# Optimization experiments

Hardware: AMD Instinct MI355X
Metric: run time of the kernel (lower is better)

Reference implementation:

```python
import jax, jax.numpy as jnp
import numpy as np

N = 64          # num_nodes (EEG electrodes)
T = 200         # time steps
B = 64          # batch
H = 64          # hidden_dim
K = 3           # cheb_k
F_IN = 1        # input_dim
D_GRU = 2 * H * N  # 8192, GRU input size


def setup_inputs() -> dict:
    key = jax.random.key(0)
    ks = jax.random.split(key, 24)
    s = 0.05
    inp = {
        "x": jax.random.normal(ks[0], (B, N, T), dtype=jnp.float32),
        "spatial_ei": jax.random.randint(ks[1], (2, 512), 0, N, dtype=jnp.int32),
        "spatial_ew": jax.random.uniform(ks[2], (512,), dtype=jnp.float32),
        "functional_ei": jax.random.randint(ks[3], (2, 1024), 0, N, dtype=jnp.int32),
        "functional_ew": jax.random.uniform(ks[4], (1024,), dtype=jnp.float32),
        # ChebConv: K separate Linear(F_IN->H, bias shared once)
        "Wcheb": jax.random.normal(ks[5], (K, F_IN, H), dtype=jnp.float32) * s,
        "bcheb": jnp.zeros((H,), jnp.float32),
        # GCNConv
        "Wgcn": jax.random.normal(ks[6], (F_IN, H), dtype=jnp.float32) * s,
        "bgcn": jnp.zeros((H,), jnp.float32),
        # bidirectional GRU (torch layout: gates r,z,n stacked -> 3H rows)
        "Wih_f": jax.random.normal(ks[7], (3 * H, D_GRU), dtype=jnp.float32) * s,
        "Whh_f": jax.random.normal(ks[8], (3 * H, H), dtype=jnp.float32) * s,
        "bih_f": jnp.zeros((3 * H,), jnp.float32),
        "bhh_f": jnp.zeros((3 * H,), jnp.float32),
        "Wih_b": jax.random.normal(ks[9], (3 * H, D_GRU), dtype=jnp.float32) * s,
        "Whh_b": jax.random.normal(ks[10], (3 * H, H), dtype=jnp.float32) * s,
        "bih_b": jnp.zeros((3 * H,), jnp.float32),
        "bhh_b": jnp.zeros((3 * H,), jnp.float32),
        # attention + classifier heads
        "attn_W": jax.random.normal(ks[11], (2 * H, 1), dtype=jnp.float32) * s,
        "attn_b": jnp.zeros((1,), jnp.float32),
        "clf_W": jax.random.normal(ks[12], (2 * H, 1), dtype=jnp.float32) * s,
        "clf_b": jnp.zeros((1,), jnp.float32),
    }
    return inp


def _gru_scan(xp, Whh, bhh, reverse):
    # xp: [B, T, 3H] precomputed input projection; returns [B, T, H]
    xp_t = jnp.swapaxes(xp, 0, 1)  # [T, B, 3H]
    Hh = Whh.shape[1]

    def step(h, xg):
        hg = h @ Whh.T + bhh
        xr, xz, xn = jnp.split(xg, 3, axis=-1)
        hr, hz, hn = jnp.split(hg, 3, axis=-1)
        r = jax.nn.sigmoid(xr + hr)
        z = jax.nn.sigmoid(xz + hz)
        n = jnp.tanh(xn + r * hn)
        h_new = (1.0 - z) * n + z * h
        return h_new, h_new

    h0 = jnp.zeros((xp.shape[0], Hh), xp.dtype)
    _, hs = jax.lax.scan(step, h0, xp_t, reverse=reverse)
    return jnp.swapaxes(hs, 0, 1)


def _forward(x, spatial_ei, spatial_ew, functional_ei, functional_ew,
             Wcheb, bcheb, Wgcn, bgcn,
             Wih_f, Whh_f, bih_f, bhh_f, Wih_b, Whh_b, bih_b, bhh_b,
             attn_W, attn_b, clf_W, clf_b):
    x = x[..., None]  # [B, N, T, 1] (the x.dim()==3 -> unsqueeze path)
    Bsz, Nn, Tt, _ = x.shape

    # ---- ChebConv (PyG, sym norm, lambda_max=2): L_tilde = -D^-1/2 A D^-1/2
    # (scaled-Laplacian self loops cancel: 2*1/2 - 1 = 0)
    row, col = spatial_ei[0], spatial_ei[1]
    deg = jax.ops.segment_sum(spatial_ew, row, num_segments=Nn)
    dinv = jnp.where(deg > 0, jax.lax.rsqrt(jnp.where(deg > 0, deg, 1.0)), 0.0)
    wn = dinv[row] * spatial_ew * dinv[col]
    # operator S[i, j]: aggregate source j into target i (source_to_target flow)
    S = jnp.zeros((Nn, Nn), x.dtype).at[col, row].add(wn)
    Ltil = -S
    Tx0 = x
    Tx1 = jnp.einsum('ij,bjtf->bitf', Ltil, Tx0)
    out_s = jnp.einsum('bntf,fh->bnth', Tx0, Wcheb[0]) + jnp.einsum('bntf,fh->bnth', Tx1, Wcheb[1])
    for k in range(2, K):
        Tx2 = 2.0 * jnp.einsum('ij,bjtf->bitf', Ltil, Tx1) - Tx0
        out_s = out_s + jnp.einsum('bntf,fh->bnth', Tx2, Wcheb[k])
        Tx0, Tx1 = Tx1, Tx2
    h_sp = out_s + bcheb  # [B, N, T, H]

    # ---- GCNConv (PyG gcn_norm with self loops, weight 1)
    row, col = functional_ei[0], functional_ei[1]
    deg = jax.ops.segment_sum(functional_ew, col, num_segments=Nn) + 1.0
    dinv = jax.lax.rsqrt(deg)
    wn = dinv[row] * functional_ew * dinv[col]
    Sg = jnp.zeros((Nn, Nn), x.dtype).at[col, row].add(wn) + jnp.diag(dinv * dinv)
    h_fn = jnp.einsum('bntf,fh->bnth', jnp.einsum('ij,bjtf->bitf', Sg, x), Wgcn) + bgcn

    # ---- stack over time, flatten nodes
    h = jnp.concatenate([h_sp, h_fn], axis=-1)           # [B, N, T, 2H]
    gru_in = jnp.transpose(h, (0, 2, 1, 3)).reshape(Bsz, Tt, Nn * 2 * H)

    # ---- bidirectional GRU
    xp_f = jnp.einsum('btd,gd->btg', gru_in, Wih_f) + bih_f
    xp_b = jnp.einsum('btd,gd->btg', gru_in, Wih_b) + bih_b
    h_f = _gru_scan(xp_f, Whh_f, bhh_f, reverse=False)
    h_b = _gru_scan(xp_b, Whh_b, bhh_b, reverse=True)
    gru_out = jnp.concatenate([h_f, h_b], axis=-1)       # [B, T, 2H]

    # ---- attention pooling + classifier
    scores = jnp.tanh(gru_out @ attn_W + attn_b)         # [B, T, 1]
    aw = jax.nn.softmax(scores, axis=1)
    ctx = jnp.sum(aw * gru_out, axis=1)                  # [B, 2H]
    return jax.nn.sigmoid(ctx @ clf_W + clf_b)           # [B, 1]


def reference(x, spatial_ei, spatial_ew, functional_ei, functional_ew,
              Wcheb, bcheb, Wgcn, bgcn,
              Wih_f, Whh_f, bih_f, bhh_f, Wih_b, Whh_b, bih_b, bhh_b,
              attn_W, attn_b, clf_W, clf_b):
    return _forward(x, spatial_ei, spatial_ew, functional_ei, functional_ew,
                    Wcheb, bcheb, Wgcn, bgcn,
                    Wih_f, Whh_f, bih_f, bhh_f, Wih_b, Whh_b, bih_b, bhh_b,
                    attn_W, attn_b, clf_W, clf_b)
```

## Files before the change

kernel.cpp:

```cpp
#include <hip/hip_runtime.h>
#include <math.h>

#define Nn 64
#define Tt 200
#define Bb 64

__device__ __forceinline__ float sigm(float x){ return 1.0f/(1.0f+__expf(-x)); }
__device__ __forceinline__ float tanh_fast(float x){
  x = fminf(fmaxf(x, -15.f), 15.f);
  float e = __expf(-2.f*x);
  return (1.f - e)/(1.f + e);
}

typedef __attribute__((ext_vector_type(4))) float f4;

__global__ __launch_bounds__(256) void k1_graphs(
    const int* __restrict__ sp_ei, const float* __restrict__ sp_ew,
    const int* __restrict__ fn_ei, const float* __restrict__ fn_ew,
    float* __restrict__ Lg, float* __restrict__ L2g, float* __restrict__ Gm)
{
  __shared__ float deg[Nn];
  __shared__ float dinv[Nn];
  __shared__ float S[64*68];
  const int tid = threadIdx.x;

  if (tid < Nn) deg[tid] = 0.f;
  for (int i=tid;i<64*68;i+=256) S[i]=0.f;
  __syncthreads();
  for (int e=tid;e<512;e+=256) atomicAdd(&deg[sp_ei[e]], sp_ew[e]);
  __syncthreads();
  if (tid < Nn) dinv[tid] = (deg[tid] > 0.f) ? rsqrtf(deg[tid]) : 0.f;
  __syncthreads();
  for (int e=tid;e<512;e+=256) {
    int r = sp_ei[e], c = sp_ei[512+e];
    atomicAdd(&S[c*68 + r], dinv[r]*sp_ew[e]*dinv[c]);
  }
  __syncthreads();
  for (int i=tid;i<4096;i+=256) Lg[i] = -S[(i>>6)*68 + (i&63)];
  {
    const int n = tid>>2, mb = (tid&3)*16;
    float a[16];
    #pragma unroll
    for (int q=0;q<16;q++) a[q]=0.f;
    for (int j=0;j<64;j++){
      float snj = S[n*68+j];
      const float4* rj = (const float4*)&S[j*68+mb];
      #pragma unroll
      for (int q=0;q<4;q++){
        float4 v = rj[q];
        a[q*4+0]=fmaf(snj,v.x,a[q*4+0]);
        a[q*4+1]=fmaf(snj,v.y,a[q*4+1]);
        a[q*4+2]=fmaf(snj,v.z,a[q*4+2]);
        a[q*4+3]=fmaf(snj,v.w,a[q*4+3]);
      }
    }
    #pragma unroll
    for (int q=0;q<16;q++){
      int m = mb+q;
      L2g[n*64+m] = 2.f*a[q] - (n==m ? 1.f : 0.f);
    }
  }
  __syncthreads();

  if (tid < Nn) deg[tid] = 0.f;
  for (int i=tid;i<64*68;i+=256) S[i]=0.f;
  __syncthreads();
  for (int e=tid;e<1024;e+=256) atomicAdd(&deg[fn_ei[1024+e]], fn_ew[e]);
  __syncthreads();
  if (tid < Nn) dinv[tid] = rsqrtf(deg[tid] + 1.f);
  __syncthreads();
  for (int e=tid;e<1024;e+=256) {
    int r = fn_ei[e], c = fn_ei[1024+e];
    atomicAdd(&S[c*68 + r], dinv[r]*fn_ew[e]*dinv[c]);
  }
  __syncthreads();
  if (tid < Nn) S[tid*68 + tid] += dinv[tid]*dinv[tid];
  __syncthreads();
  for (int i=tid;i<4096;i+=256) Gm[i] = S[(i>>6)*68 + (i&63)];
}

__global__ __launch_bounds__(64) void k2_aeff(
    const float* __restrict__ Wih_f, const float* __restrict__ bih_f,
    const float* __restrict__ Wih_b, const float* __restrict__ bih_b,
    const float* __restrict__ Wcheb, const float* __restrict__ bcheb,
    const float* __restrict__ Wgcn,  const float* __restrict__ bgcn,
    const float* __restrict__ Lg, const float* __restrict__ L2g,
    const float* __restrict__ Gm,
    float* __restrict__ Aeff, float* __restrict__ constv)
{
  const int g = blockIdx.x;
  const int dir = (g >= 192) ? 1 : 0;
  const int grow = dir ? g - 192 : g;
  const float* Wih = dir ? Wih_b : Wih_f;
  const float* bih = dir ? bih_b : bih_f;

  __shared__ float wrow[64*129];
  __shared__ float arow[256];
  const int tid = threadIdx.x;

  for (int i = tid; i < 8192; i += 64)
    wrow[(i>>7)*129 + (i&127)] = Wih[grow*8192 + i];
  __syncthreads();

  const int n = tid;
  float a0=0.f,a1=0.f,a2=0.f,a3=0.f,cp=0.f;
  for (int c=0;c<64;c++) {
    float w1 = wrow[n*129 + c];
    a0 = fmaf(w1, Wcheb[c],     a0);
    a1 = fmaf(w1, Wcheb[64+c],  a1);
    a2 = fmaf(w1, Wcheb[128+c], a2);
    cp = fmaf(w1, bcheb[c],     cp);
    float w2 = wrow[n*129 + 64 + c];
    a3 = fmaf(w2, Wgcn[c], a3);
    cp = fmaf(w2, bgcn[c], cp);
  }
  arow[n*4+0]=a0; arow[n*4+1]=a1; arow[n*4+2]=a2; arow[n*4+3]=a3;
  for (int off=32; off; off>>=1) cp += __shfl_down(cp, off, 64);
  if (tid==0) constv[g] = cp + bih[grow];
  __syncthreads();

  const int m = tid;
  float ae = arow[m*4+0];
  for (int nn2=0; nn2<64; nn2++) {
    ae = fmaf(arow[nn2*4+1], Lg [nn2*64+m], ae);
    ae = fmaf(arow[nn2*4+2], L2g[nn2*64+m], ae);
    ae = fmaf(arow[nn2*4+3], Gm [nn2*64+m], ae);
  }
  Aeff[g*64+m] = ae;
}

__global__ __launch_bounds__(256) void k3_transpose(
    const float* __restrict__ x, float* __restrict__ xTr)
{
  const int b = blockIdx.x;
  for (int idx = threadIdx.x; idx < Tt*Nn; idx += 256) {
    int t = idx >> 6, m = idx & 63;
    xTr[(b*Tt + t)*64 + m] = x[(b*64 + m)*Tt + t];
  }
}

__global__ __launch_bounds__(256) void k4_gemm(
    const float* __restrict__ xTr, const float* __restrict__ Aeff,
    const float* __restrict__ constv, float* __restrict__ xp)
{
  const int m0 = blockIdx.x*64, g0 = blockIdx.y*64;
  __shared__ float sX[64*68];
  __shared__ float sA[64*68];
  const int tid = threadIdx.x;
  const float4* xTr4 = (const float4*)xTr;
  const float4* A4   = (const float4*)Aeff;

  #pragma unroll
  for (int i=0;i<4;i++) {
    int f = tid + i*256;
    int row = f >> 4, kq = f & 15;
    float4 v = xTr4[(m0+row)*16 + kq];
    float vv[4] = {v.x,v.y,v.z,v.w};
    float4 w = A4[(g0+row)*16 + kq];
    float wv[4] = {w.x,w.y,w.z,w.w};
    #pragma unroll
    for (int q=0;q<4;q++) {
      sX[(kq*4+q)*68 + row] = vv[q];
      sA[(kq*4+q)*68 + row] = wv[q];
    }
  }
  __syncthreads();

  const int tm = tid & 15, tn = tid >> 4;
  float acc[4][4] = {};
  #pragma unroll 8
  for (int k=0;k<64;k++) {
    float4 a  = *(const float4*)&sX[k*68 + tm*4];
    float4 bb = *(const float4*)&sA[k*68 + tn*4];
    float av[4]={a.x,a.y,a.z,a.w}, bv[4]={bb.x,bb.y,bb.z,bb.w};
    #pragma unroll
    for (int i=0;i<4;i++)
      #pragma unroll
      for (int j=0;j<4;j++)
        acc[i][j] = fmaf(av[i], bv[j], acc[i][j]);
  }

  float cv[4];
  #pragma unroll
  for (int j=0;j<4;j++) cv[j] = constv[g0 + tn*4 + j];
  #pragma unroll
  for (int i=0;i<4;i++) {
    int mrow = m0 + tm*4 + i;
    #pragma unroll
    for (int j=0;j<4;j++)
      xp[mrow*384 + g0 + tn*4 + j] = acc[i][j] + cv[j];
  }
}

__global__ __launch_bounds__(192, 1) void k5_gru(
    const float* __restrict__ xp,
    const float* __restrict__ Whh_f, const float* __restrict__ bhh_f,
    const float* __restrict__ Whh_b, const float* __restrict__ bhh_b,
    float* __restrict__ gru_out)
{
  const int bd = blockIdx.x;
  const int b = bd >> 1, dir = bd & 1;
  const int g = threadIdx.x;
  const float* Whh = dir ? Whh_b : Whh_f;
  const float* bhh = dir ? bhh_b : bhh_f;

  f4 w[16];
  #pragma unroll
  for (int j=0;j<16;j++) w[j] = ((const f4*)(Whh + g*64))[j];
  const float bh = bhh[g];

  __shared__ __align__(16) float h_s[64];
  __shared__ float hg_s[192];
  __shared__ float xn_s[64];
  const f4* h4 = (const f4*)h_s;

  float hprev = 0.f;
  if (g < 64) h_s[g] = 0.f;

  const int t0 = dir ? (Tt-1) : 0;
  const int tstep = dir ? -1 : 1;
  const float* xbase = xp + ((size_t)b*Tt)*384 + dir*192 + g;
  float* gout = gru_out + ((size_t)b*Tt)*128 + dir*64 + g;

  float xqA = xbase[(size_t)t0*384];
  float xqB = xbase[(size_t)(t0+tstep)*384];
  __syncthreads();

  int t = t0;
  auto STEP = [&](float& xq) {
    float a0=0.f,a1=0.f,a2=0.f,a3=0.f;
    #pragma unroll
    for (int j=0;j<4;j++){
      f4 w0=w[4*j], w1=w[4*j+1], w2=w[4*j+2], w3=w[4*j+3];
      f4 h0=h4[4*j], h1=h4[4*j+1], h2=h4[4*j+2], h3=h4[4*j+3];
      a0=fmaf(w0.x,h0.x,a0); a0=fmaf(w0.y,h0.y,a0); a0=fmaf(w0.z,h0.z,a0); a0=fmaf(w0.w,h0.w,a0);
      a1=fmaf(w1.x,h1.x,a1); a1=fmaf(w1.y,h1.y,a1); a1=fmaf(w1.z,h1.z,a1); a1=fmaf(w1.w,h1.w,a1);
      a2=fmaf(w2.x,h2.x,a2); a2=fmaf(w2.y,h2.y,a2); a2=fmaf(w2.z,h2.z,a2); a2=fmaf(w2.w,h2.w,a2);
      a3=fmaf(w3.x,h3.x,a3); a3=fmaf(w3.y,h3.y,a3); a3=fmaf(w3.z,h3.z,a3); a3=fmaf(w3.w,h3.w,a3);
    }
    float pre = ((a0+a1)+(a2+a3)) + bh;
    if (g < 128) pre += xq;
    else xn_s[g-128] = xq;
    hg_s[g] = pre;

    int tpre = t + 2*tstep;
    if ((unsigned)tpre < (unsigned)Tt) xq = xbase[(size_t)tpre*384];

    __syncthreads();
    if (g < 64) {
      float r   = sigm(hg_s[g]);
      float z   = sigm(hg_s[64+g]);
      float nng = tanh_fast(xn_s[g] + r*hg_s[128+g]);
      float hnew = (1.f-z)*nng + z*hprev;
      hprev = hnew;
      h_s[g] = hnew;
      gout[(size_t)t*128] = hnew;
    }
    __syncthreads();
    t += tstep;
  };

  for (int sp=0; sp<Tt; sp+=2) {
    STEP(xqA);
    STEP(xqB);
  }
}

__global__ __launch_bounds__(256) void k6_attn(
    const float* __restrict__ gru_out,
    const float* __restrict__ attn_W, const float* __restrict__ attn_b,
    const float* __restrict__ clf_W,  const float* __restrict__ clf_b,
    float* __restrict__ out)
{
  const int b = blockIdx.x, tid = threadIdx.x;
  __shared__ float s_s[Tt];
  __shared__ float red[256];
  __shared__ float aW[128], cW[128];
  if (tid < 128) { aW[tid]=attn_W[tid]; cW[tid]=clf_W[tid]; }
  __syncthreads();

  if (tid < Tt) {
    const float* row = gru_out + (b*Tt + tid)*128;
    float acc = 0.f;
    for (int j=0;j<128;j++) acc = fmaf(row[j], aW[j], acc);
    s_s[tid] = tanhf(acc + attn_b[0]);
  }
  __syncthreads();

  red[tid] = (tid < Tt) ? s_s[tid] : -1e30f;
  __syncthreads();
  for (int s2=128;s2;s2>>=1){ if(tid<s2) red[tid]=fmaxf(red[tid],red[tid+s2]); __syncthreads(); }
  float mx = red[0];
  __syncthreads();

  float e = 0.f;
  if (tid < Tt) { e = expf(s_s[tid]-mx); s_s[tid] = e; }
  red[tid] = e;
  __syncthreads();
  for (int s2=128;s2;s2>>=1){ if(tid<s2) red[tid]+=red[tid+s2]; __syncthreads(); }
  float total = red[0];
  __syncthreads();

  float p = 0.f;
  if (tid < 128) {
    float c = 0.f;
    for (int t=0;t<Tt;t++) c = fmaf(s_s[t], gru_out[(b*Tt+t)*128 + tid], c);
    p = (c/total)*cW[tid];
  }
  red[tid] = p;
  __syncthreads();
  for (int s2=128;s2;s2>>=1){ if(tid<s2) red[tid]+=red[tid+s2]; __syncthreads(); }
  if (tid==0) out[b] = sigm(red[0] + clf_b[0]);
}

extern "C" void kernel_launch(void* const* d_in, const int* in_sizes, int n_in,
                              void* d_out, int out_size, void* d_ws, size_t ws_size,
                              hipStream_t stream)
{
  const float* x      = (const float*)d_in[0];
  const int*   sp_ei  = (const int*)  d_in[1];
  const float* sp_ew  = (const float*)d_in[2];
  const int*   fn_ei  = (const int*)  d_in[3];
  const float* fn_ew  = (const float*)d_in[4];
  const float* Wcheb  = (const float*)d_in[5];
  const float* bcheb  = (const float*)d_in[6];
  const float* Wgcn   = (const float*)d_in[7];
  const float* bgcn   = (const float*)d_in[8];
  const float* Wih_f  = (const float*)d_in[9];
  const float* Whh_f  = (const float*)d_in[10];
  const float* bih_f  = (const float*)d_in[11];
  const float* bhh_f  = (const float*)d_in[12];
  const float* Wih_b  = (const float*)d_in[13];
  const float* Whh_b  = (const float*)d_in[14];
  const float* bih_b  = (const float*)d_in[15];
  const float* bhh_b  = (const float*)d_in[16];
  const float* attn_W = (const float*)d_in[17];
  const float* attn_b = (const float*)d_in[18];
  const float* clf_W  = (const float*)d_in[19];
  const float* clf_b  = (const float*)d_in[20];
  float* out = (float*)d_out;

  float* ws     = (float*)d_ws;
  float* Lg     = ws;
  float* L2g    = Lg   + 4096;
  float* Gm     = L2g  + 4096;
  float* Aeff   = Gm   + 4096;
  float* constv = Aeff + 24576;
  float* xTr    = constv + 512;
  float* xp     = xTr  + 819200;
  float* gro    = xp   + 4915200;

  hipLaunchKernelGGL(k1_graphs,    dim3(1),      dim3(256), 0, stream,
                     sp_ei, sp_ew, fn_ei, fn_ew, Lg, L2g, Gm);
  hipLaunchKernelGGL(k3_transpose, dim3(64),     dim3(256), 0, stream, x, xTr);
  hipLaunchKernelGGL(k2_aeff,      dim3(384),    dim3(64),  0, stream,
                     Wih_f, bih_f, Wih_b, bih_b, Wcheb, bcheb, Wgcn, bgcn,
                     Lg, L2g, Gm, Aeff, constv);
  hipLaunchKernelGGL(k4_gemm,      dim3(200, 6), dim3(256), 0, stream,
                     xTr, Aeff, constv, xp);
  hipLaunchKernelGGL(k5_gru,       dim3(128),    dim3(192), 0, stream,
                     xp, Whh_f, bhh_f, Whh_b, bhh_b, gro);
  hipLaunchKernelGGL(k6_attn,      dim3(64),     dim3(256), 0, stream,
                     gro, attn_W, attn_b, clf_W, clf_b, out);
}
```

Baseline: 164.0 us.

## Run GRU recurrence in a single wavefront with fp16 dot2 and readlane broadcast

The GRU kernel moves from 192 threads with shared-memory exchange and two barriers per step to one 64-lane wavefront per (batch, direction). Each lane owns one hidden unit and holds its r, z and n weight rows in registers as packed fp16 pairs. The hidden state is broadcast through shuffle and readlane, and the dot products use the fdot2 instruction. This removes the per-step barriers and LDS round trips on the serial critical path, at the cost of fp16 precision for the recurrent weights and state and a smaller 64-thread block.

Result: slower. 169.0 us (+3.0%).

```diff
diff --git a/kernel.cpp b/kernel.cpp
--- a/kernel.cpp
+++ b/kernel.cpp
@@ -12,7 +12,14 @@
   return (1.f - e)/(1.f + e);
 }
 
+typedef __attribute__((ext_vector_type(2))) _Float16 h2v;
 typedef __attribute__((ext_vector_type(4))) float f4;
+
+#if __has_builtin(__builtin_amdgcn_fdot2)
+#define DOT2(w,hv,acc) __builtin_amdgcn_fdot2((w),(hv),(acc),false)
+#else
+#define DOT2(w,hv,acc) fmaf((float)(w)[0],(float)(hv)[0], fmaf((float)(w)[1],(float)(hv)[1],(acc)))
+#endif
 
 __global__ __launch_bounds__(256) void k1_graphs(
     const int* __restrict__ sp_ei, const float* __restrict__ sp_ew,
@@ -192,7 +199,7 @@
   }
 }
 
-__global__ __launch_bounds__(192, 1) void k5_gru(
+__global__ __launch_bounds__(64, 1) void k5_gru(
     const float* __restrict__ xp,
     const float* __restrict__ Whh_f, const float* __restrict__ bhh_f,
     const float* __restrict__ Whh_b, const float* __restrict__ bhh_b,
@@ -200,70 +207,67 @@
 {
   const int bd = blockIdx.x;
   const int b = bd >> 1, dir = bd & 1;
-  const int g = threadIdx.x;
+  const int g = threadIdx.x & 63;
   const float* Whh = dir ? Whh_b : Whh_f;
   const float* bhh = dir ? bhh_b : bhh_f;
 
-  f4 w[16];
+  h2v wr[32], wz[32], wn[32];
   #pragma unroll
-  for (int j=0;j<16;j++) w[j] = ((const f4*)(Whh + g*64))[j];
-  const float bh = bhh[g];
-
-  __shared__ __align__(16) float h_s[64];
-  __shared__ float hg_s[192];
-  __shared__ float xn_s[64];
-  const f4* h4 = (const f4*)h_s;
-
-  float hprev = 0.f;
-  if (g < 64) h_s[g] = 0.f;
+  for (int i=0;i<32;i++){
+    float2 a = ((const float2*)(Whh + (size_t)g*64))[i];
+    float2 bq= ((const float2*)(Whh + (size_t)(64+g)*64))[i];
+    float2 c = ((const float2*)(Whh + (size_t)(128+g)*64))[i];
+    wr[i] = h2v{(_Float16)a.x, (_Float16)a.y};
+    wz[i] = h2v{(_Float16)bq.x,(_Float16)bq.y};
+    wn[i] = h2v{(_Float16)c.x, (_Float16)c.y};
+  }
+  const float br_ = bhh[g], bz_ = bhh[64+g], bn_ = bhh[128+g];
 
   const int t0 = dir ? (Tt-1) : 0;
   const int tstep = dir ? -1 : 1;
-  const float* xbase = xp + ((size_t)b*Tt)*384 + dir*192 + g;
-  float* gout = gru_out + ((size_t)b*Tt)*128 + dir*64 + g;
-
-  float xqA = xbase[(size_t)t0*384];
-  float xqB = xbase[(size_t)(t0+tstep)*384];
-  __syncthreads();
+  const float* xb = xp + (size_t)(b*Tt)*384 + dir*192 + g;
+  float* gout = gru_out + (size_t)(b*Tt)*128 + dir*64 + g;
+
+  float h = 0.f;
+  float xrA = xb[(size_t)t0*384], xzA = xb[(size_t)t0*384+64], xnA = xb[(size_t)t0*384+128];
+  const int t1 = t0 + tstep;
+  float xrB = xb[(size_t)t1*384], xzB = xb[(size_t)t1*384+64], xnB = xb[(size_t)t1*384+128];
 
   int t = t0;
-  auto STEP = [&](float& xq) {
-    float a0=0.f,a1=0.f,a2=0.f,a3=0.f;
-    #pragma unroll
-    for (int j=0;j<4;j++){
-      f4 w0=w[4*j], w1=w[4*j+1], w2=w[4*j+2], w3=w[4*j+3];
-      f4 h0=h4[4*j], h1=h4[4*j+1], h2=h4[4*j+2], h3=h4[4*j+3];
-      a0=fmaf(w0.x,h0.x,a0); a0=fmaf(w0.y,h0.y,a0); a0=fmaf(w0.z,h0.z,a0); a0=fmaf(w0.w,h0.w,a0);
-      a1=fmaf(w1.x,h1.x,a1); a1=fmaf(w1.y,h1.y,a1); a1=fmaf(w1.z,h1.z,a1); a1=fmaf(w1.w,h1.w,a1);
-      a2=fmaf(w2.x,h2.x,a2); a2=fmaf(w2.y,h2.y,a2); a2=fmaf(w2.z,h2.z,a2); a2=fmaf(w2.w,h2.w,a2);
-      a3=fmaf(w3.x,h3.x,a3); a3=fmaf(w3.y,h3.y,a3); a3=fmaf(w3.z,h3.z,a3); a3=fmaf(w3.w,h3.w,a3);
-    }
-    float pre = ((a0+a1)+(a2+a3)) + bh;
-    if (g < 128) pre += xq;
-    else xn_s[g-128] = xq;
-    hg_s[g] = pre;
-
-    int tpre = t + 2*tstep;
-    if ((unsigned)tpre < (unsigned)Tt) xq = xbase[(size_t)tpre*384];
-
-    __syncthreads();
-    if (g < 64) {
-      float r   = sigm(hg_s[g]);
-      float z   = sigm(hg_s[64+g]);
-      float nng = tanh_fast(xn_s[g] + r*hg_s[128+g]);
-      float hnew = (1.f-z)*nng + z*hprev;
-      hprev = hnew;
-      h_s[g] = hnew;
-      gout[(size_t)t*128] = hnew;
-    }
-    __syncthreads();
+  auto STEP = [&](float& xr, float& xz, float& xn){
+    float nb = __shfl_xor(h, 1, 64);
+    h2v hp; hp[0] = (_Float16)h; hp[1] = (_Float16)nb;
+    const int hpk = __builtin_bit_cast(int, hp);
+
+    float ar0=0.f,ar1=0.f,az0=0.f,az1=0.f,an0=0.f,an1=0.f;
+    #pragma unroll
+    for (int i=0;i<32;i+=2){
+      int p0 = __builtin_amdgcn_readlane(hpk, 2*i);
+      int p1 = __builtin_amdgcn_readlane(hpk, 2*i+2);
+      h2v h0 = __builtin_bit_cast(h2v, p0);
+      h2v h1 = __builtin_bit_cast(h2v, p1);
+      ar0 = DOT2(wr[i],  h0, ar0);  az0 = DOT2(wz[i],  h0, az0);  an0 = DOT2(wn[i],  h0, an0);
+      ar1 = DOT2(wr[i+1],h1, ar1);  az1 = DOT2(wz[i+1],h1, az1);  an1 = DOT2(wn[i+1],h1, an1);
+    }
+
+    const float cxr = xr, cxz = xz, cxn = xn;
+    const int tpre = t + 2*tstep;
+    if ((unsigned)tpre < (unsigned)Tt) {
+      xr = xb[(size_t)tpre*384];
+      xz = xb[(size_t)tpre*384+64];
+      xn = xb[(size_t)tpre*384+128];
+    }
+
+    float r   = sigm(cxr + (ar0+ar1) + br_);
+    float z   = sigm(cxz + (az0+az1) + bz_);
+    float nn2 = tanh_fast(cxn + r*((an0+an1) + bn_));
+    float hnew = (1.f - z)*nn2 + z*h;
+    h = hnew;
+    gout[(size_t)t*128] = hnew;
     t += tstep;
   };
 
-  for (int sp=0; sp<Tt; sp+=2) {
-    STEP(xqA);
-    STEP(xqB);
-  }
+  for (int sp=0; sp<Tt; sp+=2) { STEP(xrA,xzA,xnA); STEP(xrB,xzB,xnB); }
 }
 
 __global__ __launch_bounds__(256) void k6_attn(
@@ -358,7 +362,7 @@
                      Lg, L2g, Gm, Aeff, constv);
   hipLaunchKernelGGL(k4_gemm,      dim3(200, 6), dim3(256), 0, stream,
                      xTr, Aeff, constv, xp);
-  hipLaunchKernelGGL(k5_gru,       dim3(128),    dim3(192), 0, stream,
+  hipLaunchKernelGGL(k5_gru,       dim3(128),    dim3(64),  0, stream,
                      xp, Whh_f, bhh_f, Whh_b, bhh_b, gro);
   hipLaunchKernelGGL(k6_attn,      dim3(64),     dim3(256), 0, stream,
                      gro, attn_W, attn_b, clf_W, clf_b, out);
```
